# Kernel tuning notes

Hardware: AMD Instinct MI355X
Metric: run time of the kernel (lower is better)

Reference implementation:

```python
import jax, jax.numpy as jnp
import numpy as np
from jax import lax

N, L, D, F = 16, 512, 256, 256
KW = 3
EPS = 1e-5


def setup_inputs() -> dict:
    key = jax.random.key(0)
    ks = jax.random.split(key, 12)
    return {
        "x": jax.random.normal(ks[0], (N, L, D), jnp.float32),
        "conv1_w": jax.random.normal(ks[1], (F, D, KW), jnp.float32) * 0.05,
        "conv1_b": jnp.zeros((F,), jnp.float32),
        "ln1_g": jnp.ones((F,), jnp.float32),
        "ln1_b": jnp.zeros((F,), jnp.float32),
        "conv2_w": jax.random.normal(ks[2], (F, F, KW), jnp.float32) * 0.05,
        "conv2_b": jnp.zeros((F,), jnp.float32),
        "ln2_g": jnp.ones((F,), jnp.float32),
        "ln2_b": jnp.zeros((F,), jnp.float32),
        "lin_w": jax.random.normal(ks[3], (F, 1), jnp.float32) * 0.05,
        "lin_b": jnp.zeros((1,), jnp.float32),
        "target": jax.random.randint(ks[4], (N, L), 1, 8, jnp.int32),
        "mel_max_length": 4096,
    }


def _layernorm(h, g, b):
    m = jnp.mean(h, axis=-1, keepdims=True)
    v = jnp.var(h, axis=-1, keepdims=True)
    return (h - m) * lax.rsqrt(v + EPS) * g + b


def _conv1d(h, w, b):
    # h: [N, L, C_in]; w: [C_out, C_in, K]; 'same' padding=1 for K=3
    y = lax.conv_general_dilated(h.transpose(0, 2, 1), w, (1,), [(1, 1)],
                                 dimension_numbers=("NCH", "OIH", "NCH"))
    return (y + b[None, :, None]).transpose(0, 2, 1)


def _duration_predictor(x, c1w, c1b, g1, b1, c2w, c2b, g2, b2, lw, lb):
    h = jax.nn.relu(_layernorm(_conv1d(x, c1w, c1b), g1, b1))
    h = jax.nn.relu(_layernorm(_conv1d(h, c2w, c2b), g2, b2))
    return jax.nn.relu(h @ lw + lb)[..., 0]  # [N, L]


def _length_regulate(x, dur, T):
    # Equivalent to one-hot alignment @ x, done as a duration-indexed gather.
    cum = jnp.cumsum(dur, axis=-1)                       # [N, L]
    t = jnp.arange(T, dtype=cum.dtype)                   # [T]
    idx = jax.vmap(lambda c: jnp.searchsorted(c, t, side="right"))(cum)  # [N, T]
    valid = t[None, :] < cum[:, -1:]                     # [N, T]
    out = jnp.take_along_axis(x, jnp.clip(idx, 0, x.shape[1] - 1)[:, :, None], axis=1)
    return jnp.where(valid[..., None], out, jnp.zeros((), x.dtype))


def reference(x, conv1_w, conv1_b, ln1_g, ln1_b, conv2_w, conv2_b, ln2_g, ln2_b,
              lin_w, lin_b, target, mel_max_length):
    dpo = _duration_predictor(x, conv1_w, conv1_b, ln1_g, ln1_b,
                              conv2_w, conv2_b, ln2_g, ln2_b, lin_w, lin_b)
    out = _length_regulate(x, target, mel_max_length)    # [N, mel_max_length, D]
    return (out, dpo)
```

## Files before the change

kernel.cpp:

```cpp
#include <hip/hip_runtime.h>
#include <hip/hip_bf16.h>

using u16 = unsigned short;
typedef __bf16 bf16x8 __attribute__((ext_vector_type(8)));
typedef float f32x4 __attribute__((ext_vector_type(4)));

#define N_B   16
#define L_S   512
#define D_F   256
#define T_MEL 4096
#define M_TOT (N_B * L_S)
#define OUT_ELEMS ((size_t)N_B * T_MEL * D_F)
#define H1_ELEMS  ((size_t)M_TOT * D_F)
#define WP_ELEMS  (24 * 8192)
#define TBLK 128

__device__ __forceinline__ u16 f2bf(float f) {
  __hip_bfloat16 h = __float2bfloat16(f);
  return *(u16*)&h;
}

__device__ __forceinline__ bf16x8 pack8(float4 v0, float4 v1) {
  union { bf16x8 h; u16 u[8]; } r;
  r.u[0] = f2bf(v0.x); r.u[1] = f2bf(v0.y); r.u[2] = f2bf(v0.z); r.u[3] = f2bf(v0.w);
  r.u[4] = f2bf(v1.x); r.u[5] = f2bf(v1.y); r.u[6] = f2bf(v1.z); r.u[7] = f2bf(v1.w);
  return r.h;
}

__global__ __launch_bounds__(256)
void pack_kernel(const float* __restrict__ w1, const float* __restrict__ w2,
                 u16* __restrict__ wp1, u16* __restrict__ wp2) {
  int o   = (int)blockIdx.x * 256 + (int)threadIdx.x;
  int s   = o >> 13;
  int rem = o & 8191;
  int f   = rem >> 5;
  int ki  = rem & 31;
  int d   = ((s & 7) << 5) + ki;
  int tap = s >> 3;
  int src = f * 768 + d * 3 + tap;
  wp1[o] = f2bf(w1[src]);
  wp2[o] = f2bf(w2[src]);
}

template<int STAGE>
__device__ __forceinline__ void conv_body_dir(
    const int blk, const int t,
    const float* __restrict__ Xf, const u16* __restrict__ Xh,
    const u16* __restrict__ Wp,
    const float* __restrict__ cb,  const float* __restrict__ lgm,
    const float* __restrict__ lbt, const float* __restrict__ lw,
    const float* __restrict__ lb,  u16* __restrict__ Hout,
    float* __restrict__ dpo,
    u16* As, float* sBias, float* sG, float* sB, float* sLw,
    float (*redS)[4][16], float (*redQ)[4][16])
{
  if (t < 256) {
    sBias[t] = cb[t];
    sG[t]    = lgm[t];
    sB[t]    = lbt[t];
    if (STAGE == 2) sLw[t] = lw[t];
  }

  const int m0   = blk * 32;
  const int n    = m0 >> 9;
  const int l0   = m0 & 511;
  const int wave = t >> 6, lane = t & 63;
  const int cs   = wave & 3;
  const int rh   = wave >> 2;
  const int wc   = cs * 64;
  const int rh16 = rh * 16;
  const int p    = lane & 15, q = lane >> 4;

  f32x4 acc[4];
  #pragma unroll
  for (int i = 0; i < 4; i++) acc[i] = (f32x4){0.f, 0.f, 0.f, 0.f};

  for (int c = t; c < 1088; c += 512) {
    int row  = c >> 5;
    int col8 = c & 31;
    int l    = l0 + row - 1;
    uint4 val;
    if ((unsigned)l < 512u) {
      if (STAGE == 1) {
        const float* src = Xf + (((size_t)((n << 9) + l)) << 8) + (col8 << 3);
        float4 v0 = *(const float4*)src;
        float4 v1 = *(const float4*)(src + 4);
        bf16x8 pk = pack8(v0, v1);
        __builtin_memcpy(&val, &pk, 16);
      } else {
        val = *(const uint4*)(Xh + (((size_t)((n << 9) + l)) << 8) + (col8 << 3));
      }
    } else {
      val = make_uint4(0u, 0u, 0u, 0u);
    }
    *(uint4*)(As + row * 264 + (col8 << 3)) = val;
  }
  __syncthreads();

  const u16* wbase = Wp + ((wc + p) << 5) + (q << 3);
  auto LDB = [&](int s, bf16x8 (&b)[4]) {
    const u16* src = wbase + ((size_t)s << 13);
    #pragma unroll
    for (int ct = 0; ct < 4; ct++)
      b[ct] = *(const bf16x8*)(src + (ct << 9));
  };
  auto MF = [&](int s, bf16x8 (&b)[4]) {
    const int tap = s >> 3, dbase = (s & 7) << 5;
    bf16x8 af = *(const bf16x8*)(As + (rh16 + p + tap) * 264 + dbase + (q << 3));
    #pragma unroll
    for (int ct = 0; ct < 4; ct++)
      acc[ct] = __builtin_amdgcn_mfma_f32_16x16x32_bf16(af, b[ct], acc[ct], 0, 0, 0);
  };

  bf16x8 bA[4], bB[4], bC[4];
  LDB(0, bA);
  LDB(1, bB);
  for (int s3 = 0; s3 < 24; s3 += 3) {
    LDB(s3 + 2, bC);
    MF(s3, bA);
    if (s3 + 3 < 24) LDB(s3 + 3, bA);
    MF(s3 + 1, bB);
    if (s3 + 4 < 24) LDB(s3 + 4, bB);
    MF(s3 + 2, bC);
    if (s3 + 5 < 24) LDB(s3 + 5, bC);
  }

  float s0[4] = {0,0,0,0}, s1[4] = {0,0,0,0};
  #pragma unroll
  for (int ct = 0; ct < 4; ct++) {
    float bias = sBias[wc + ct * 16 + p];
    #pragma unroll
    for (int j = 0; j < 4; j++) {
      float v = acc[ct][j] + bias;
      acc[ct][j] = v;
      s0[j] += v;
      s1[j] += v * v;
    }
  }
  #pragma unroll
  for (int m = 1; m <= 8; m <<= 1) {
    #pragma unroll
    for (int j = 0; j < 4; j++) {
      s0[j] += __shfl_xor(s0[j], m);
      s1[j] += __shfl_xor(s1[j], m);
    }
  }
  if (p == 0) {
    #pragma unroll
    for (int j = 0; j < 4; j++) {
      redS[rh][cs][q * 4 + j] = s0[j];
      redQ[rh][cs][q * 4 + j] = s1[j];
    }
  }
  __syncthreads();
  float mean[4], rstd[4];
  #pragma unroll
  for (int j = 0; j < 4; j++) {
    int r = q * 4 + j;
    float S = redS[rh][0][r] + redS[rh][1][r] + redS[rh][2][r] + redS[rh][3][r];
    float Q = redQ[rh][0][r] + redQ[rh][1][r] + redQ[rh][2][r] + redQ[rh][3][r];
    float mu  = S * (1.0f / 256.0f);
    float var = Q * (1.0f / 256.0f) - mu * mu;
    mean[j] = mu;
    rstd[j] = rsqrtf(var + 1e-5f);
  }

  if (STAGE == 1) {
    #pragma unroll
    for (int ct = 0; ct < 4; ct++) {
      int c = wc + ct * 16 + p;
      float gg = sG[c], bb = sB[c];
      #pragma unroll
      for (int j = 0; j < 4; j++) {
        float v = (acc[ct][j] - mean[j]) * rstd[j] * gg + bb;
        v = fmaxf(v, 0.0f);
        Hout[(size_t)(m0 + rh16 + q * 4 + j) * 256 + c] = f2bf(v);
      }
    }
  } else {
    float ls[4] = {0,0,0,0};
    #pragma unroll
    for (int ct = 0; ct < 4; ct++) {
      int c = wc + ct * 16 + p;
      float gg = sG[c], bb = sB[c], ww = sLw[c];
      #pragma unroll
      for (int j = 0; j < 4; j++) {
        float v = (acc[ct][j] - mean[j]) * rstd[j] * gg + bb;
        v = fmaxf(v, 0.0f);
        ls[j] += v * ww;
      }
    }
    #pragma unroll
    for (int m = 1; m <= 8; m <<= 1) {
      #pragma unroll
      for (int j = 0; j < 4; j++) ls[j] += __shfl_xor(ls[j], m);
    }
    __syncthreads();
    if (p == 0) {
      #pragma unroll
      for (int j = 0; j < 4; j++) redS[rh][cs][q * 4 + j] = ls[j];
    }
    __syncthreads();
    if (t < 32) {
      int r2 = t >> 4, ri = t & 15;
      float dv = fmaxf(redS[r2][0][ri] + redS[r2][1][ri] +
                       redS[r2][2][ri] + redS[r2][3][ri] + lb[0], 0.0f);
      dpo[m0 + t] = dv;
    }
  }
}

__device__ __forceinline__ void lr_body512(
    const int lrblk, const int t,
    const float* __restrict__ X, const int* __restrict__ tgt,
    float* __restrict__ out, int* sc, int* sidx)
{
  const int n  = lrblk >> 4;
  const int t0 = (lrblk & 15) * 256;

  sc[t] = tgt[n * L_S + t];
  __syncthreads();
  for (int off = 1; off < L_S; off <<= 1) {
    int v = (t >= off) ? sc[t - off] : 0;
    __syncthreads();
    sc[t] += v;
    __syncthreads();
  }
  const int total = sc[L_S - 1];
  if (t < 256) {
    int tt = t0 + t;
    int lo = 0, hi = L_S;
    while (lo < hi) {
      int mid = (lo + hi) >> 1;
      if (sc[mid] <= tt) lo = mid + 1; else hi = mid;
    }
    sidx[t] = (tt < total) ? lo : -1;
  }
  __syncthreads();

  #pragma unroll
  for (int i = 0; i < 32; i++) {
    int u   = t + i * 512;
    int dg  = u & 63;
    int tr  = u >> 6;
    int idx = sidx[tr];
    float4 v = make_float4(0.f, 0.f, 0.f, 0.f);
    if (idx >= 0)
      v = *(const float4*)(X + (((size_t)(n * L_S + idx)) << 8) + dg * 4);
    *(float4*)(out + (((size_t)(n * T_MEL + t0 + tr)) << 8) + dg * 4) = v;
  }
}

template<int STAGE>
__global__ __launch_bounds__(512)
void conv_dir_kernel(const float* __restrict__ Xf, const u16* __restrict__ Xh,
                     const u16* __restrict__ Wp,
                     const float* __restrict__ cb,  const float* __restrict__ lgm,
                     const float* __restrict__ lbt, const float* __restrict__ lw,
                     const float* __restrict__ lb,  u16* __restrict__ Hout,
                     float* __restrict__ dpo)
{
  __shared__ __align__(16) u16 As[34 * 264 + 8];
  __shared__ float sBias[256], sG[256], sB[256], sLw[256];
  __shared__ float redS[2][4][16], redQ[2][4][16];
  conv_body_dir<STAGE>((int)blockIdx.x, (int)threadIdx.x, Xf, Xh, Wp, cb, lgm,
                       lbt, lw, lb, Hout, dpo, As, sBias, sG, sB, sLw, redS, redQ);
}

__global__ __launch_bounds__(512)
void conv1_lr_dir_kernel(const float* __restrict__ x, const u16* __restrict__ Wp,
                         const float* __restrict__ cb,  const float* __restrict__ lgm,
                         const float* __restrict__ lbt, u16* __restrict__ Hout,
                         const int* __restrict__ tgt, float* __restrict__ out)
{
  __shared__ __align__(16) u16 As[34 * 264 + 8];
  __shared__ float sBias[256], sG[256], sB[256], sLw[256];
  __shared__ float redS[2][4][16], redQ[2][4][16];
  __shared__ int  sc[512];
  __shared__ int  sidx[256];

  const int blk = (int)blockIdx.x, t = (int)threadIdx.x;
  if (blk < 256) {
    conv_body_dir<1>(blk, t, x, nullptr, Wp, cb, lgm, lbt, nullptr, nullptr,
                     Hout, nullptr, As, sBias, sG, sB, sLw, redS, redQ);
  } else {
    lr_body512(blk - 256, t, x, tgt, out, sc, sidx);
  }
}

template<int STAGE>
__device__ __forceinline__ void conv_body(
    const int blk, const int t,
    const float* __restrict__ Xf, const u16* __restrict__ Xh,
    const u16* __restrict__ Wp,
    const float* __restrict__ cb,  const float* __restrict__ lgm,
    const float* __restrict__ lbt, const float* __restrict__ lw,
    const float* __restrict__ lb,  u16* __restrict__ Hout,
    float* __restrict__ dpo,
    u16* As, u16* Bs, float* sBias, float* sG, float* sB, float* sLw,
    float (*redS)[4][16], float (*redQ)[4][16])
{
  if (t < 256) {
    sBias[t] = cb[t];
    sG[t]    = lgm[t];
    sB[t]    = lbt[t];
    if (STAGE == 2) sLw[t] = lw[t];
  }

  const int m0   = blk * 32;
  const int n    = m0 >> 9;
  const int l0   = m0 & 511;
  const int wave = t >> 6, lane = t & 63;
  const int cs   = wave & 3;
  const int rh   = wave >> 2;
  const int wc   = cs * 64;
  const int rh16 = rh * 16;
  const int p    = lane & 15, q = lane >> 4;

  f32x4 acc[4];
  #pragma unroll
  for (int i = 0; i < 4; i++) acc[i] = (f32x4){0.f, 0.f, 0.f, 0.f};

  auto LDW = [&](int s, uint4 &r0, uint4 &r1) {
    const u16* src = Wp + ((size_t)s << 13);
    r0 = *(const uint4*)(src + (t << 3));
    r1 = *(const uint4*)(src + ((t + 512) << 3));
  };
  auto WRB = [&](int buf, const uint4 &r0, const uint4 &r1) {
    *(uint4*)(Bs + (buf << 13) + (t << 3))         = r0;
    *(uint4*)(Bs + (buf << 13) + ((t + 512) << 3)) = r1;
  };
  auto MF = [&](int buf, int s) {
    const u16* bs = Bs + (buf << 13);
    const int tap = s >> 3, dbase = (s & 7) << 5;
    bf16x8 af = *(const bf16x8*)(As + (rh16 + p + tap) * 264 + dbase + (q << 3));
    #pragma unroll
    for (int ct = 0; ct < 4; ct++) {
      bf16x8 bfr = *(const bf16x8*)(bs + ((wc + ct * 16 + p) << 5) + (q << 3));
      acc[ct] = __builtin_amdgcn_mfma_f32_16x16x32_bf16(af, bfr, acc[ct], 0, 0, 0);
    }
  };

  uint4 e0, e1, o0, o1;
  LDW(0, e0, e1);
  LDW(1, o0, o1);

  for (int c = t; c < 1088; c += 512) {
    int row  = c >> 5;
    int col8 = c & 31;
    int l    = l0 + row - 1;
    uint4 val;
    if ((unsigned)l < 512u) {
      if (STAGE == 1) {
        const float* src = Xf + (((size_t)((n << 9) + l)) << 8) + (col8 << 3);
        float4 v0 = *(const float4*)src;
        float4 v1 = *(const float4*)(src + 4);
        bf16x8 pk = pack8(v0, v1);
        __builtin_memcpy(&val, &pk, 16);
      } else {
        val = *(const uint4*)(Xh + (((size_t)((n << 9) + l)) << 8) + (col8 << 3));
      }
    } else {
      val = make_uint4(0u, 0u, 0u, 0u);
    }
    *(uint4*)(As + row * 264 + (col8 << 3)) = val;
  }
  WRB(0, e0, e1);
  __syncthreads();

  for (int s2 = 0; s2 < 24; s2 += 2) {
    MF(0, s2);
    if (s2 + 2 < 24) LDW(s2 + 2, e0, e1);
    WRB(1, o0, o1);
    __syncthreads();
    MF(1, s2 + 1);
    if (s2 + 3 < 24) LDW(s2 + 3, o0, o1);
    if (s2 + 2 < 24) WRB(0, e0, e1);
    __syncthreads();
  }

  float s0[4] = {0,0,0,0}, s1[4] = {0,0,0,0};
  #pragma unroll
  for (int ct = 0; ct < 4; ct++) {
    float bias = sBias[wc + ct * 16 + p];
    #pragma unroll
    for (int j = 0; j < 4; j++) {
      float v = acc[ct][j] + bias;
      acc[ct][j] = v;
      s0[j] += v;
      s1[j] += v * v;
    }
  }
  #pragma unroll
  for (int m = 1; m <= 8; m <<= 1) {
    #pragma unroll
    for (int j = 0; j < 4; j++) {
      s0[j] += __shfl_xor(s0[j], m);
      s1[j] += __shfl_xor(s1[j], m);
    }
  }
  if (p == 0) {
    #pragma unroll
    for (int j = 0; j < 4; j++) {
      redS[rh][cs][q * 4 + j] = s0[j];
      redQ[rh][cs][q * 4 + j] = s1[j];
    }
  }
  __syncthreads();
  float mean[4], rstd[4];
  #pragma unroll
  for (int j = 0; j < 4; j++) {
    int r = q * 4 + j;
    float S = redS[rh][0][r] + redS[rh][1][r] + redS[rh][2][r] + redS[rh][3][r];
    float Q = redQ[rh][0][r] + redQ[rh][1][r] + redQ[rh][2][r] + redQ[rh][3][r];
    float mu  = S * (1.0f / 256.0f);
    float var = Q * (1.0f / 256.0f) - mu * mu;
    mean[j] = mu;
    rstd[j] = rsqrtf(var + 1e-5f);
  }

  if (STAGE == 1) {
    #pragma unroll
    for (int ct = 0; ct < 4; ct++) {
      int c = wc + ct * 16 + p;
      float gg = sG[c], bb = sB[c];
      #pragma unroll
      for (int j = 0; j < 4; j++) {
        float v = (acc[ct][j] - mean[j]) * rstd[j] * gg + bb;
        v = fmaxf(v, 0.0f);
        Hout[(size_t)(m0 + rh16 + q * 4 + j) * 256 + c] = f2bf(v);
      }
    }
  } else {
    float ls[4] = {0,0,0,0};
    #pragma unroll
    for (int ct = 0; ct < 4; ct++) {
      int c = wc + ct * 16 + p;
      float gg = sG[c], bb = sB[c], ww = sLw[c];
      #pragma unroll
      for (int j = 0; j < 4; j++) {
        float v = (acc[ct][j] - mean[j]) * rstd[j] * gg + bb;
        v = fmaxf(v, 0.0f);
        ls[j] += v * ww;
      }
    }
    #pragma unroll
    for (int m = 1; m <= 8; m <<= 1) {
      #pragma unroll
      for (int j = 0; j < 4; j++) ls[j] += __shfl_xor(ls[j], m);
    }
    __syncthreads();
    if (p == 0) {
      #pragma unroll
      for (int j = 0; j < 4; j++) redS[rh][cs][q * 4 + j] = ls[j];
    }
    __syncthreads();
    if (t < 32) {
      int r2 = t >> 4, ri = t & 15;
      float dv = fmaxf(redS[r2][0][ri] + redS[r2][1][ri] +
                       redS[r2][2][ri] + redS[r2][3][ri] + lb[0], 0.0f);
      dpo[m0 + t] = dv;
    }
  }
}

template<int STAGE>
__global__ __launch_bounds__(512)
void conv_ln_kernel(const float* __restrict__ Xf, const u16* __restrict__ Xh,
                    const u16* __restrict__ Wp,
                    const float* __restrict__ cb,  const float* __restrict__ lgm,
                    const float* __restrict__ lbt, const float* __restrict__ lw,
                    const float* __restrict__ lb,  u16* __restrict__ Hout,
                    float* __restrict__ dpo)
{
  __shared__ __align__(16) u16 As[34 * 264 + 8];
  __shared__ __align__(16) u16 Bs[2 * 8192];
  __shared__ float sBias[256], sG[256], sB[256], sLw[256];
  __shared__ float redS[2][4][16], redQ[2][4][16];
  conv_body<STAGE>((int)blockIdx.x, (int)threadIdx.x, Xf, Xh, Wp, cb, lgm, lbt,
                   lw, lb, Hout, dpo, As, Bs, sBias, sG, sB, sLw, redS, redQ);
}

__global__ __launch_bounds__(256)
void lr_kernel(const float* __restrict__ X, const int* __restrict__ tgt,
               float* __restrict__ out) {
  __shared__ int c[L_S];
  __shared__ int sidx[TBLK];
  const int t  = threadIdx.x;
  const int n  = blockIdx.x >> 5;
  const int t0 = (blockIdx.x & 31) * TBLK;

  c[t]       = tgt[n * L_S + t];
  c[t + 256] = tgt[n * L_S + t + 256];
  __syncthreads();
  for (int off = 1; off < L_S; off <<= 1) {
    int v0 = (t >= off) ? c[t - off] : 0;
    int i1 = t + 256;
    int v1 = (i1 >= off) ? c[i1 - off] : 0;
    __syncthreads();
    c[t]  += v0;
    c[i1] += v1;
    __syncthreads();
  }
  const int total = c[L_S - 1];
  if (t < TBLK) {
    int tt = t0 + t;
    int lo = 0, hi = L_S;
    while (lo < hi) {
      int mid = (lo + hi) >> 1;
      if (c[mid] <= tt) lo = mid + 1; else hi = mid;
    }
    sidx[t] = (tt < total) ? lo : -1;
  }
  __syncthreads();

  #pragma unroll
  for (int i = 0; i < 32; i++) {
    int u   = t + i * 256;
    int dg  = u & 63;
    int tr  = u >> 6;
    int idx = sidx[tr];
    float4 v = make_float4(0.f, 0.f, 0.f, 0.f);
    if (idx >= 0)
      v = *(const float4*)(X + (((size_t)(n * L_S + idx)) << 8) + dg * 4);
    *(float4*)(out + (((size_t)(n * T_MEL + t0 + tr)) << 8) + dg * 4) = v;
  }
}

extern "C" void kernel_launch(void* const* d_in, const int* in_sizes, int n_in,
                              void* d_out, int out_size, void* d_ws, size_t ws_size,
                              hipStream_t stream) {
  (void)in_sizes; (void)n_in; (void)out_size;

  const float* x   = (const float*)d_in[0];
  const float* w1  = (const float*)d_in[1];
  const float* b1  = (const float*)d_in[2];
  const float* g1  = (const float*)d_in[3];
  const float* be1 = (const float*)d_in[4];
  const float* w2  = (const float*)d_in[5];
  const float* b2  = (const float*)d_in[6];
  const float* g2  = (const float*)d_in[7];
  const float* be2 = (const float*)d_in[8];
  const float* lw  = (const float*)d_in[9];
  const float* lb  = (const float*)d_in[10];
  const int*   tgt = (const int*)d_in[11];

  float* out = (float*)d_out;
  float* dpo = out + OUT_ELEMS;

  const size_t need = (H1_ELEMS + 2 * (size_t)WP_ELEMS) * sizeof(u16);

  if (d_ws != nullptr && ws_size >= need) {
    u16* h1  = (u16*)d_ws;
    u16* wp1 = h1 + H1_ELEMS;
    u16* wp2 = wp1 + WP_ELEMS;
    pack_kernel<<<768, 256, 0, stream>>>(w1, w2, wp1, wp2);
    conv1_lr_dir_kernel<<<512, 512, 0, stream>>>(x, wp1, b1, g1, be1, h1, tgt, out);
    conv_dir_kernel<2><<<M_TOT / 32, 512, 0, stream>>>(
        nullptr, h1, wp2, b2, g2, be2, lw, lb, nullptr, dpo);
  } else {
    u16* h1  = (u16*)d_out;
    u16* wp1 = h1 + H1_ELEMS;
    u16* wp2 = wp1 + WP_ELEMS;
    pack_kernel<<<768, 256, 0, stream>>>(w1, w2, wp1, wp2);
    conv_ln_kernel<1><<<M_TOT / 32, 512, 0, stream>>>(
        x, nullptr, wp1, b1, g1, be1, nullptr, nullptr, h1, nullptr);
    conv_ln_kernel<2><<<M_TOT / 32, 512, 0, stream>>>(
        nullptr, h1, wp2, b2, g2, be2, lw, lb, nullptr, dpo);
    lr_kernel<<<N_B * (T_MEL / TBLK), 256, 0, stream>>>(x, tgt, out);
  }
}
```

Measured before the change: 133.3 us.

## Stage conv weights into LDS via global_load_lds double buffering

Replaces per-wave register-prefetched global weight loads in the conv GEMM with direct global-to-LDS async loads (global_load_lds) into a double-buffered shared tile. Each K-step's weight slab is loaded once per block and shared across the two row-halves of waves, cutting redundant global/L2 traffic. The cost is two block-wide barriers per pair of steps, an extra 32KB of LDS per block that may reduce occupancy, and LDS read traffic for B fragments. The kernel is dominated by the large length-regulate output write, so the conv portion is a limited fraction of the total.

```diff
diff --git a/kernel.cpp b/kernel.cpp
--- a/kernel.cpp
+++ b/kernel.cpp
@@ -43,7 +43,7 @@
 }
 
 template<int STAGE>
-__device__ __forceinline__ void conv_body_dir(
+__device__ __forceinline__ void conv_body_gll(
     const int blk, const int t,
     const float* __restrict__ Xf, const u16* __restrict__ Xh,
     const u16* __restrict__ Wp,
@@ -51,7 +51,7 @@
     const float* __restrict__ lbt, const float* __restrict__ lw,
     const float* __restrict__ lb,  u16* __restrict__ Hout,
     float* __restrict__ dpo,
-    u16* As, float* sBias, float* sG, float* sB, float* sLw,
+    u16* As, u16* Bs, float* sBias, float* sG, float* sB, float* sLw,
     float (*redS)[4][16], float (*redQ)[4][16])
 {
   if (t < 256) {
@@ -70,10 +70,35 @@
   const int wc   = cs * 64;
   const int rh16 = rh * 16;
   const int p    = lane & 15, q = lane >> 4;
+  const int wv64 = wave << 6;
 
   f32x4 acc[4];
   #pragma unroll
   for (int i = 0; i < 4; i++) acc[i] = (f32x4){0.f, 0.f, 0.f, 0.f};
+
+  auto GLL = [&](int s, int buf) {
+    const u16* src = Wp + ((size_t)s << 13);
+    __builtin_amdgcn_global_load_lds(
+        (const __attribute__((address_space(1))) void*)(src + (t << 3)),
+        (__attribute__((address_space(3))) void*)(Bs + (buf << 13) + (wv64 << 3)),
+        16, 0, 0);
+    __builtin_amdgcn_global_load_lds(
+        (const __attribute__((address_space(1))) void*)(src + ((t + 512) << 3)),
+        (__attribute__((address_space(3))) void*)(Bs + (buf << 13) + ((wv64 + 512) << 3)),
+        16, 0, 0);
+  };
+  auto MF = [&](int buf, int s) {
+    const u16* bs = Bs + (buf << 13);
+    const int tap = s >> 3, dbase = (s & 7) << 5;
+    bf16x8 af = *(const bf16x8*)(As + (rh16 + p + tap) * 264 + dbase + (q << 3));
+    #pragma unroll
+    for (int ct = 0; ct < 4; ct++) {
+      bf16x8 bfr = *(const bf16x8*)(bs + ((wc + ct * 16 + p) << 5) + (q << 3));
+      acc[ct] = __builtin_amdgcn_mfma_f32_16x16x32_bf16(af, bfr, acc[ct], 0, 0, 0);
+    }
+  };
+
+  GLL(0, 0);
 
   for (int c = t; c < 1088; c += 512) {
     int row  = c >> 5;
@@ -97,32 +122,13 @@
   }
   __syncthreads();
 
-  const u16* wbase = Wp + ((wc + p) << 5) + (q << 3);
-  auto LDB = [&](int s, bf16x8 (&b)[4]) {
-    const u16* src = wbase + ((size_t)s << 13);
-    #pragma unroll
-    for (int ct = 0; ct < 4; ct++)
-      b[ct] = *(const bf16x8*)(src + (ct << 9));
-  };
-  auto MF = [&](int s, bf16x8 (&b)[4]) {
-    const int tap = s >> 3, dbase = (s & 7) << 5;
-    bf16x8 af = *(const bf16x8*)(As + (rh16 + p + tap) * 264 + dbase + (q << 3));
-    #pragma unroll
-    for (int ct = 0; ct < 4; ct++)
-      acc[ct] = __builtin_amdgcn_mfma_f32_16x16x32_bf16(af, b[ct], acc[ct], 0, 0, 0);
-  };
-
-  bf16x8 bA[4], bB[4], bC[4];
-  LDB(0, bA);
-  LDB(1, bB);
-  for (int s3 = 0; s3 < 24; s3 += 3) {
-    LDB(s3 + 2, bC);
-    MF(s3, bA);
-    if (s3 + 3 < 24) LDB(s3 + 3, bA);
-    MF(s3 + 1, bB);
-    if (s3 + 4 < 24) LDB(s3 + 4, bB);
-    MF(s3 + 2, bC);
-    if (s3 + 5 < 24) LDB(s3 + 5, bC);
+  for (int s2 = 0; s2 < 24; s2 += 2) {
+    GLL(s2 + 1, 1);
+    MF(0, s2);
+    __syncthreads();
+    if (s2 + 2 < 24) GLL(s2 + 2, 0);
+    MF(1, s2 + 1);
+    __syncthreads();
   }
 
   float s0[4] = {0,0,0,0}, s1[4] = {0,0,0,0};
@@ -253,7 +259,7 @@
 
 template<int STAGE>
 __global__ __launch_bounds__(512)
-void conv_dir_kernel(const float* __restrict__ Xf, const u16* __restrict__ Xh,
+void conv_gll_kernel(const float* __restrict__ Xf, const u16* __restrict__ Xh,
                      const u16* __restrict__ Wp,
                      const float* __restrict__ cb,  const float* __restrict__ lgm,
                      const float* __restrict__ lbt, const float* __restrict__ lw,
@@ -261,19 +267,22 @@
                      float* __restrict__ dpo)
 {
   __shared__ __align__(16) u16 As[34 * 264 + 8];
+  __shared__ __align__(16) u16 Bs[2 * 8192];
   __shared__ float sBias[256], sG[256], sB[256], sLw[256];
   __shared__ float redS[2][4][16], redQ[2][4][16];
-  conv_body_dir<STAGE>((int)blockIdx.x, (int)threadIdx.x, Xf, Xh, Wp, cb, lgm,
-                       lbt, lw, lb, Hout, dpo, As, sBias, sG, sB, sLw, redS, redQ);
+  conv_body_gll<STAGE>((int)blockIdx.x, (int)threadIdx.x, Xf, Xh, Wp, cb, lgm,
+                       lbt, lw, lb, Hout, dpo, As, Bs, sBias, sG, sB, sLw,
+                       redS, redQ);
 }
 
 __global__ __launch_bounds__(512)
-void conv1_lr_dir_kernel(const float* __restrict__ x, const u16* __restrict__ Wp,
+void conv1_lr_gll_kernel(const float* __restrict__ x, const u16* __restrict__ Wp,
                          const float* __restrict__ cb,  const float* __restrict__ lgm,
                          const float* __restrict__ lbt, u16* __restrict__ Hout,
                          const int* __restrict__ tgt, float* __restrict__ out)
 {
   __shared__ __align__(16) u16 As[34 * 264 + 8];
+  __shared__ __align__(16) u16 Bs[2 * 8192];
   __shared__ float sBias[256], sG[256], sB[256], sLw[256];
   __shared__ float redS[2][4][16], redQ[2][4][16];
   __shared__ int  sc[512];
@@ -281,8 +290,8 @@
 
   const int blk = (int)blockIdx.x, t = (int)threadIdx.x;
   if (blk < 256) {
-    conv_body_dir<1>(blk, t, x, nullptr, Wp, cb, lgm, lbt, nullptr, nullptr,
-                     Hout, nullptr, As, sBias, sG, sB, sLw, redS, redQ);
+    conv_body_gll<1>(blk, t, x, nullptr, Wp, cb, lgm, lbt, nullptr, nullptr,
+                     Hout, nullptr, As, Bs, sBias, sG, sB, sLw, redS, redQ);
   } else {
     lr_body512(blk - 256, t, x, tgt, out, sc, sidx);
   }
@@ -555,8 +564,8 @@
     u16* wp1 = h1 + H1_ELEMS;
     u16* wp2 = wp1 + WP_ELEMS;
     pack_kernel<<<768, 256, 0, stream>>>(w1, w2, wp1, wp2);
-    conv1_lr_dir_kernel<<<512, 512, 0, stream>>>(x, wp1, b1, g1, be1, h1, tgt, out);
-    conv_dir_kernel<2><<<M_TOT / 32, 512, 0, stream>>>(
+    conv1_lr_gll_kernel<<<512, 512, 0, stream>>>(x, wp1, b1, g1, be1, h1, tgt, out);
+    conv_gll_kernel<2><<<M_TOT / 32, 512, 0, stream>>>(
         nullptr, h1, wp2, b2, g2, be2, lw, lb, nullptr, dpo);
   } else {
     u16* h1  = (u16*)d_out;
```

Result: faster. 129.8 us (-2.6%).
